# Performance work log

Hardware: AMD Instinct MI355X
Metric: run time of the kernel (lower is better)

## Reference

```python
import jax, jax.numpy as jnp
import numpy as np

N_CORES = 64
N_QUBITS = 1024
QEMB = 256
N_EDGES = 448
BATCH = 512
NN_DIMS = (256, 512, 512, 256)


def setup_inputs() -> dict:
    key = jax.random.key(0)
    ks = jax.random.split(key, 12)
    inp = {
        "core_allocs": jax.random.randint(ks[0], (BATCH, N_QUBITS), 0, N_CORES, dtype=jnp.int32),
        "qubit_embs": jax.random.normal(ks[1], (N_QUBITS, QEMB), dtype=jnp.float32),
        "dummy_qubit_emb": jax.random.normal(ks[2], (QEMB,), dtype=jnp.float32),
        "edge_index": jax.random.randint(ks[3], (2, N_EDGES), 0, N_CORES, dtype=jnp.int32),
        "edge_weight": jax.random.uniform(ks[4], (N_EDGES,), dtype=jnp.float32),
        "W1": jax.random.normal(ks[5], (NN_DIMS[0], NN_DIMS[1]), dtype=jnp.float32) * 0.05,
        "b1": jax.random.normal(ks[6], (NN_DIMS[1],), dtype=jnp.float32) * 0.05,
        "W2": jax.random.normal(ks[7], (NN_DIMS[1], NN_DIMS[2]), dtype=jnp.float32) * 0.05,
        "b2": jax.random.normal(ks[8], (NN_DIMS[2],), dtype=jnp.float32) * 0.05,
        "W3": jax.random.normal(ks[9], (NN_DIMS[2], NN_DIMS[3]), dtype=jnp.float32) * 0.05,
        "b3": jax.random.normal(ks[10], (NN_DIMS[3],), dtype=jnp.float32) * 0.05,
    }
    return inp


def _gcn_norm(edge_index, edge_weight):
    # PyG gcn_norm: add self loops (weight 1), symmetric D^{-1/2} A D^{-1/2}.
    self_idx = jnp.arange(N_CORES, dtype=edge_index.dtype)
    row = jnp.concatenate([edge_index[0], self_idx])
    col = jnp.concatenate([edge_index[1], self_idx])
    w = jnp.concatenate([edge_weight, jnp.ones((N_CORES,), edge_weight.dtype)])
    deg = jax.ops.segment_sum(w, col, num_segments=N_CORES)  # degree at targets
    dinv = jnp.where(deg > 0, deg ** -0.5, 0.0)
    norm = dinv[row] * w * dinv[col]
    return row, col, norm


def reference(core_allocs, qubit_embs, dummy_qubit_emb, edge_index, edge_weight,
              W1, b1, W2, b2, W3, b3):
    # ---- unmixedCoreEmbs, vectorized: per-core max over assigned qubit embs,
    # dummy emb always included (cores never at capacity) ----
    def pool(alloc):  # alloc: [n_qubits] -> [n_cores, qemb]
        seg = jax.ops.segment_max(qubit_embs, alloc, num_segments=N_CORES)
        return jnp.maximum(seg, dummy_qubit_emb)  # also fixes -inf empty cores

    x = jax.vmap(pool)(core_allocs)  # [B, n_cores, qemb]

    # ---- GCNConv stack (same graph replicated per batch element) ----
    row, col, norm = _gcn_norm(edge_index, edge_weight)

    def gcn_layer(h, W, b):
        hw = h @ W  # [B, C, d_out]
        msg = hw[:, row, :] * norm[None, :, None]  # gather sources, scale
        agg = jnp.zeros((h.shape[0], N_CORES, W.shape[1]), hw.dtype).at[:, col, :].add(msg)
        return jax.nn.relu(agg + b)

    x = gcn_layer(x, W1, b1)
    x = gcn_layer(x, W2, b2)
    x = gcn_layer(x, W3, b3)
    return x  # [B, n_cores, nn_dims[-1]] (original returns this split per batch element)
```

## Files before the change

### kernel.cpp

```cpp
#include <hip/hip_runtime.h>
#include <type_traits>

typedef __attribute__((ext_vector_type(8))) short short8;
typedef __attribute__((ext_vector_type(4))) short short4v;
typedef __attribute__((ext_vector_type(4))) float f32x4;
typedef unsigned short u16;
typedef unsigned int u32;

#define N_EDGES 448

#define WS_ADJA 0
#define WS_ADJB 4096
#define WS_W1   8192
#define WS_W2   139264
#define WS_W3   401408
#define WS_DUM  532480
#define WS_B1   (WS_DUM + 256)
#define WS_B2   (WS_DUM + 768)
#define WS_B3   (WS_DUM + 1280)
#define WS_FLAG 534272

__device__ __forceinline__ float bf2f(u16 v) {
    u32 u = ((u32)v) << 16;
    return __builtin_bit_cast(float, u);
}
__device__ __forceinline__ u16 f2bf(float f) {
    u32 u = __builtin_bit_cast(u32, f);
    u32 r = u + 0x7FFFu + ((u >> 16) & 1u);
    return (u16)(r >> 16);
}
__device__ __forceinline__ float ldf(const void* p, int idx, u32 isf32) {
    return isf32 ? ((const float*)p)[idx] : bf2f(((const u16*)p)[idx]);
}

__global__ __launch_bounds__(512) void prep(
    const int* __restrict__ eidx, const void* __restrict__ ew,
    const void* __restrict__ qembs, const void* __restrict__ dummy,
    const void* __restrict__ W1, const void* __restrict__ b1,
    const void* __restrict__ W2, const void* __restrict__ b2,
    const void* __restrict__ W3, const void* __restrict__ b3,
    u16* __restrict__ ws) {
    const int t = threadIdx.x, b = blockIdx.x;
    __shared__ u32 s_isf;
    if (t < 64) {
        const u16* qs = (const u16*)qembs;
        int c = 0;
#pragma unroll
        for (int j = 0; j < 4; j++) {
            u16 v = qs[(t * 4 + j) * 2];
            u32 e = (v >> 7) & 0xFF;
            c += (e >= 100 && e <= 134) ? 1 : 0;
        }
#pragma unroll
        for (int off = 32; off > 0; off >>= 1) c += __shfl_down(c, off, 64);
        if (t == 0) s_isf = (c < 128) ? 1u : 0u;
    }
    __syncthreads();
    const u32 isf32 = s_isf;

    if (b == 0) {
#pragma unroll
        for (int j = 0; j < 4; j++) {
            int i = t + j * 512;
            if (i < 1792) {
                float v;
                if (i < 256)       v = ldf(dummy, i, isf32);
                else if (i < 768)  v = ldf(b1, i - 256, isf32);
                else if (i < 1280) v = ldf(b2, i - 768, isf32);
                else               v = ldf(b3, i - 1280, isf32);
                ws[WS_DUM + i] = f2bf(v);
            }
        }
        __shared__ float A[4096];
        __shared__ float deg[64];
        __shared__ float dinv[64];
        __shared__ int er[N_EDGES];
        __shared__ int ec[N_EDGES];
        __shared__ float ewf[N_EDGES];
        if (t < N_EDGES) {
            er[t] = eidx[t];
            ec[t] = eidx[N_EDGES + t];
            ewf[t] = ldf(ew, t, isf32);
        }
        if (t < 64) deg[t] = 1.0f;
        for (int i = t; i < 4096; i += 512) A[i] = 0.f;
        __syncthreads();
        if (t < N_EDGES) atomicAdd(&deg[ec[t]], ewf[t]);
        __syncthreads();
        if (t < 64) dinv[t] = 1.0f / sqrtf(deg[t]);
        __syncthreads();
        if (t < N_EDGES) atomicAdd(&A[ec[t] * 64 + er[t]], dinv[er[t]] * ewf[t] * dinv[ec[t]]);
        __syncthreads();
        if (t < 64) A[t * 64 + t] += dinv[t] * dinv[t];
        __syncthreads();
        for (int i = t; i < 4096; i += 512) {
            int chunk = i >> 9, m = (i >> 3) & 63, j = i & 7;
            ws[WS_ADJA + i] = f2bf(A[m * 64 + chunk * 8 + j]);
        }
        for (int i = t; i < 4096; i += 512) {
            int chunk = i >> 9, l = (i >> 3) & 63, j = i & 7;
            int ntc = chunk >> 1, kk = chunk & 1;
            int k = kk * 32 + (l >> 4) * 8 + j;
            int c2 = ntc * 16 + (l & 15);
            ws[WS_ADJB + i] = f2bf(A[c2 * 64 + k]);
        }
        if (t == 0) *(u32*)(ws + WS_FLAG) = isf32;
    } else {
        const int bw = (b - 1) * 8 + (t >> 6);
        const int tl = t & 63;
        const void* src;
        int N, K32, dst, nt, kk;
        if (bw < 256)      { src = W1; N = 512; K32 = 8;  dst = WS_W1; nt = bw / 8;          kk = bw % 8; }
        else if (bw < 768) { src = W2; N = 512; K32 = 16; dst = WS_W2; nt = (bw - 256) / 16; kk = (bw - 256) % 16; }
        else               { src = W3; N = 256; K32 = 16; dst = WS_W3; nt = (bw - 768) / 16; kk = (bw - 768) % 16; }
        const int col = nt * 16 + (tl & 15);
        const int krow = kk * 32 + (tl >> 4) * 8;
        u16 v[8];
#pragma unroll
        for (int j = 0; j < 8; j++) v[j] = f2bf(ldf(src, (krow + j) * N + col, isf32));
        u16* o = ws + dst + (nt * K32 + kk) * 512 + tl * 8;
#pragma unroll
        for (int j = 0; j < 8; j++) o[j] = v[j];
    }
}

__global__ __launch_bounds__(1024, 4) void fused(
    const int* __restrict__ allocs, const void* __restrict__ qembs,
    const u16* __restrict__ wsr, void* __restrict__ out) {

    __shared__ __align__(16) u16 BH1[32768];
    __shared__ __align__(16) u16 BH2[32768];
    __shared__ __align__(16) u16 SCR[10240];

    const int t = threadIdx.x, bb = blockIdx.x;
    const int wave = t >> 6, lane = t & 63, quad = lane >> 4, nl = lane & 15;
    const u32 isf32 = *(const u32*)(wsr + WS_FLAG);

    {
        int* AL   = (int*)SCR;
        int* LIST = (int*)SCR + 1024;
        int* CNT  = (int*)SCR + 2048;
        int* SST  = (int*)SCR + 2112;
        int* WOF  = (int*)SCR + 2176;
        if (t < 64) CNT[t] = 0;
        __syncthreads();
        const int myc = allocs[bb * 1024 + t];
        AL[t] = myc;
        atomicAdd(&CNT[myc], 1);
        __syncthreads();
        if (t < 64) {
            int v = CNT[t], s = v;
#pragma unroll
            for (int off = 1; off < 64; off <<= 1) {
                int u = __shfl_up(s, off, 64);
                if (t >= off) s += u;
            }
            SST[t] = s - v;
            WOF[t] = s - v;
        }
        __syncthreads();
        {
            int pos = atomicAdd(&WOF[myc], 1);
            LIST[pos] = t;
        }
        __syncthreads();
        float dums[4];
#pragma unroll
        for (int jj = 0; jj < 4; jj++) dums[jj] = bf2f(wsr[WS_DUM + lane * 4 + jj]);
        for (int i = 0; i < 4; i++) {
            const int c = wave * 4 + i;
            const int L = CNT[c], S = SST[c];
            float vm0 = -3.4e38f, vm1 = -3.4e38f, vm2 = -3.4e38f, vm3 = -3.4e38f;
            if (isf32) {
                const float4* qb = (const float4*)qembs;
                for (int j = 0; j < L; j++) {
                    int q = LIST[S + j];
                    float4 v = qb[q * 64 + lane];
                    vm0 = fmaxf(vm0, v.x); vm1 = fmaxf(vm1, v.y);
                    vm2 = fmaxf(vm2, v.z); vm3 = fmaxf(vm3, v.w);
                }
            } else {
                const uint2* qb = (const uint2*)qembs;
                for (int j = 0; j < L; j++) {
                    int q = LIST[S + j];
                    uint2 r = qb[q * 64 + lane];
                    vm0 = fmaxf(vm0, bf2f((u16)(r.x & 0xffff)));
                    vm1 = fmaxf(vm1, bf2f((u16)(r.x >> 16)));
                    vm2 = fmaxf(vm2, bf2f((u16)(r.y & 0xffff)));
                    vm3 = fmaxf(vm3, bf2f((u16)(r.y >> 16)));
                }
            }
            short4v p;
            p[0] = (short)f2bf(fmaxf(vm0, dums[0]));
            p[1] = (short)f2bf(fmaxf(vm1, dums[1]));
            p[2] = (short)f2bf(fmaxf(vm2, dums[2]));
            p[3] = (short)f2bf(fmaxf(vm3, dums[3]));
            *(short4v*)(BH2 + (lane >> 1) * 512 + c * 8 + (lane & 1) * 4) = p;
        }
    }
    __syncthreads();

    u16* scr = SCR + wave * 640;

    auto layerT = [&](auto K32c, const u16* __restrict__ W, const u16* __restrict__ bias,
                      const u16* __restrict__ Hin, u16* __restrict__ Hout) {
        constexpr int K32 = decltype(K32c)::value;
        const int s0 = wave * 2;
        f32x4 acc[2][4];
#pragma unroll
        for (int s = 0; s < 2; s++)
#pragma unroll
            for (int rt = 0; rt < 4; rt++) acc[s][rt] = f32x4{0.f, 0.f, 0.f, 0.f};
#pragma unroll
        for (int kk = 0; kk < K32; kk++) {
            short8 a[4], bch[2];
#pragma unroll
            for (int rt = 0; rt < 4; rt++)
                a[rt] = *(const short8*)(Hin + (kk * 4 + quad) * 512 + (rt * 16 + nl) * 8);
#pragma unroll
            for (int s = 0; s < 2; s++)
                bch[s] = *(const short8*)(W + ((s0 + s) * K32 + kk) * 512 + lane * 8);
#pragma unroll
            for (int s = 0; s < 2; s++)
#pragma unroll
                for (int rt = 0; rt < 4; rt++)
                    acc[s][rt] = __builtin_amdgcn_mfma_f32_16x16x32_bf16(a[rt], bch[s], acc[s][rt], 0, 0, 0);
        }
#pragma unroll
        for (int s = 0; s < 2; s++) {
            const int nt = s0 + s;
            f32x4 agg[4];
#pragma unroll
            for (int ntc = 0; ntc < 4; ntc++) agg[ntc] = f32x4{0.f, 0.f, 0.f, 0.f};
#pragma unroll
            for (int h = 0; h < 2; h++) {
#pragma unroll
                for (int r2 = 0; r2 < 2; r2++) {
                    f32x4 v = acc[s][2 * h + r2];
                    short4v p;
#pragma unroll
                    for (int rr = 0; rr < 4; rr++) p[rr] = (short)f2bf(v[rr]);
                    *(short4v*)(scr + nl * 40 + r2 * 16 + quad * 4) = p;
                }
                short8 hwf = *(const short8*)(scr + nl * 40 + quad * 8);
#pragma unroll
                for (int ntc = 0; ntc < 4; ntc++) {
                    short8 adjB = *(const short8*)(wsr + WS_ADJB + (ntc * 2 + h) * 512 + lane * 8);
                    agg[ntc] = __builtin_amdgcn_mfma_f32_16x16x32_bf16(hwf, adjB, agg[ntc], 0, 0, 0);
                }
            }
            float bv[4];
#pragma unroll
            for (int rr = 0; rr < 4; rr++) bv[rr] = bf2f(bias[nt * 16 + quad * 4 + rr]);
#pragma unroll
            for (int ntc = 0; ntc < 4; ntc++) {
                short4v p;
#pragma unroll
                for (int rr = 0; rr < 4; rr++)
                    p[rr] = (short)f2bf(fmaxf(agg[ntc][rr] + bv[rr], 0.f));
                *(short4v*)(Hout + (nt * 2 + (quad >> 1)) * 512 + (ntc * 16 + nl) * 8 + (quad & 1) * 4) = p;
            }
        }
    };

    auto layer3 = [&](const u16* __restrict__ W) {
        const int nt = wave;
        f32x4 acc[4];
#pragma unroll
        for (int rt = 0; rt < 4; rt++) acc[rt] = f32x4{0.f, 0.f, 0.f, 0.f};
#pragma unroll
        for (int kk = 0; kk < 16; kk++) {
            short8 a[4];
#pragma unroll
            for (int rt = 0; rt < 4; rt++)
                a[rt] = *(const short8*)(BH2 + (kk * 4 + quad) * 512 + (rt * 16 + nl) * 8);
            short8 bch = *(const short8*)(W + (nt * 16 + kk) * 512 + lane * 8);
#pragma unroll
            for (int rt = 0; rt < 4; rt++)
                acc[rt] = __builtin_amdgcn_mfma_f32_16x16x32_bf16(a[rt], bch, acc[rt], 0, 0, 0);
        }
#pragma unroll
        for (int h = 0; h < 2; h++) {
#pragma unroll
            for (int r2 = 0; r2 < 2; r2++) {
                f32x4 v = acc[2 * h + r2];
                short4v p;
#pragma unroll
                for (int rr = 0; rr < 4; rr++) p[rr] = (short)f2bf(v[rr]);
                *(short4v*)(scr + nl * 40 + r2 * 16 + quad * 4) = p;
            }
            short8 hwf = *(const short8*)(scr + nl * 40 + quad * 8);
            *(short8*)(BH1 + (nt * 2 + h) * 512 + lane * 8) = hwf;
        }
    };

    auto finalOut = [&]() {
        const int rt2 = wave & 3, nt0 = (wave >> 2) * 4;
        short8 aA[2];
#pragma unroll
        for (int h = 0; h < 2; h++)
            aA[h] = *(const short8*)(wsr + WS_ADJA + (h * 4 + quad) * 512 + (rt2 * 16 + nl) * 8);
        float* outf = (float*)out + (size_t)bb * 16384;
        u16* outu = (u16*)out + (size_t)bb * 16384;
#pragma unroll
        for (int ni = 0; ni < 4; ni++) {
            const int nt = nt0 + ni;
            short8 b0 = *(const short8*)(BH1 + (nt * 2 + 0) * 512 + lane * 8);
            short8 b1 = *(const short8*)(BH1 + (nt * 2 + 1) * 512 + lane * 8);
            f32x4 acc = f32x4{0.f, 0.f, 0.f, 0.f};
            acc = __builtin_amdgcn_mfma_f32_16x16x32_bf16(aA[0], b0, acc, 0, 0, 0);
            acc = __builtin_amdgcn_mfma_f32_16x16x32_bf16(aA[1], b1, acc, 0, 0, 0);
            const int n = nt * 16 + nl;
            const float bv = bf2f(wsr[WS_B3 + n]);
#pragma unroll
            for (int rr = 0; rr < 4; rr++) {
                const int m2 = rt2 * 16 + quad * 4 + rr;
                float val = fmaxf(acc[rr] + bv, 0.f);
                if (isf32) outf[m2 * 256 + n] = val;
                else       outu[m2 * 256 + n] = f2bf(val);
            }
        }
    };

    layerT(std::integral_constant<int, 8>{},  wsr + WS_W1, wsr + WS_B1, BH2, BH1);
    __syncthreads();
    layerT(std::integral_constant<int, 16>{}, wsr + WS_W2, wsr + WS_B2, BH1, BH2);
    __syncthreads();
    layer3(wsr + WS_W3);
    __syncthreads();
    finalOut();
}

extern "C" void kernel_launch(void* const* d_in, const int* in_sizes, int n_in,
                              void* d_out, int out_size, void* d_ws, size_t ws_size,
                              hipStream_t stream) {
    const int* allocs = (const int*)d_in[0];
    const void* qembs = d_in[1];
    const void* dummy = d_in[2];
    const int* eidx   = (const int*)d_in[3];
    const void* ew    = d_in[4];
    const void* W1 = d_in[5];
    const void* b1 = d_in[6];
    const void* W2 = d_in[7];
    const void* b2 = d_in[8];
    const void* W3 = d_in[9];
    const void* b3 = d_in[10];
    u16* ws = (u16*)d_ws;

    prep<<<129, 512, 0, stream>>>(eidx, ew, qembs, dummy, W1, b1, W2, b2, W3, b3, ws);
    fused<<<512, 1024, 0, stream>>>(allocs, qembs, ws, d_out);
}
```

Baseline: 150.4 us.

## Merge prep and fused kernels into one cooperative kernel with grid sync

Replaces the separate prep and fused launches with a single cooperative kernel. Weight repacking, qubit-embedding bf16 conversion and adjacency building are spread across all 512 blocks, followed by a grid-wide sync; if the cooperative launch fails, two plain launches are used instead. The main compute now runs with 512 threads and a single padded LDS activation buffer (stride 520) in place of two ping-pong buffers, with more work per wave. This aims to remove a launch boundary and the serial prep tail and to raise occupancy, at the cost of a grid barrier and extra in-place syncs.

```diff
diff --git a/kernel.cpp b/kernel.cpp
--- a/kernel.cpp
+++ b/kernel.cpp
@@ -1,4 +1,5 @@
 #include <hip/hip_runtime.h>
+#include <hip/hip_cooperative_groups.h>
 #include <type_traits>
 
 typedef __attribute__((ext_vector_type(8))) short short8;
@@ -8,6 +9,7 @@
 typedef unsigned int u32;
 
 #define N_EDGES 448
+#define CH 520
 
 #define WS_ADJA 0
 #define WS_ADJB 4096
@@ -18,7 +20,7 @@
 #define WS_B1   (WS_DUM + 256)
 #define WS_B2   (WS_DUM + 768)
 #define WS_B3   (WS_DUM + 1280)
-#define WS_FLAG 534272
+#define WS_QE   534528
 
 __device__ __forceinline__ float bf2f(u16 v) {
     u32 u = ((u32)v) << 16;
@@ -33,15 +35,23 @@
     return isf32 ? ((const float*)p)[idx] : bf2f(((const u16*)p)[idx]);
 }
 
-__global__ __launch_bounds__(512) void prep(
-    const int* __restrict__ eidx, const void* __restrict__ ew,
-    const void* __restrict__ qembs, const void* __restrict__ dummy,
+template <int MODE>
+__global__ __launch_bounds__(512, 4) void mega(
+    const int* __restrict__ allocs, const void* __restrict__ qembs,
+    const void* __restrict__ dummy, const int* __restrict__ eidx,
+    const void* __restrict__ ew,
     const void* __restrict__ W1, const void* __restrict__ b1,
     const void* __restrict__ W2, const void* __restrict__ b2,
     const void* __restrict__ W3, const void* __restrict__ b3,
-    u16* __restrict__ ws) {
-    const int t = threadIdx.x, b = blockIdx.x;
+    u16* __restrict__ ws, void* __restrict__ out) {
+
+    __shared__ __align__(16) u16 H[64 * CH];
+    __shared__ __align__(16) u16 SCR[8 * 640];
     __shared__ u32 s_isf;
+
+    const int t = threadIdx.x, bb = blockIdx.x;
+    const int wave = t >> 6, lane = t & 63, quad = lane >> 4, nl = lane & 15;
+
     if (t < 64) {
         const u16* qs = (const u16*)qembs;
         int c = 0;
@@ -58,95 +68,99 @@
     __syncthreads();
     const u32 isf32 = s_isf;
 
-    if (b == 0) {
-#pragma unroll
-        for (int j = 0; j < 4; j++) {
-            int i = t + j * 512;
-            if (i < 1792) {
-                float v;
-                if (i < 256)       v = ldf(dummy, i, isf32);
-                else if (i < 768)  v = ldf(b1, i - 256, isf32);
-                else if (i < 1280) v = ldf(b2, i - 768, isf32);
-                else               v = ldf(b3, i - 1280, isf32);
-                ws[WS_DUM + i] = f2bf(v);
-            }
-        }
-        __shared__ float A[4096];
-        __shared__ float deg[64];
-        __shared__ float dinv[64];
-        __shared__ int er[N_EDGES];
-        __shared__ int ec[N_EDGES];
-        __shared__ float ewf[N_EDGES];
-        if (t < N_EDGES) {
-            er[t] = eidx[t];
-            ec[t] = eidx[N_EDGES + t];
-            ewf[t] = ldf(ew, t, isf32);
-        }
-        if (t < 64) deg[t] = 1.0f;
-        for (int i = t; i < 4096; i += 512) A[i] = 0.f;
-        __syncthreads();
-        if (t < N_EDGES) atomicAdd(&deg[ec[t]], ewf[t]);
-        __syncthreads();
-        if (t < 64) dinv[t] = 1.0f / sqrtf(deg[t]);
-        __syncthreads();
-        if (t < N_EDGES) atomicAdd(&A[ec[t] * 64 + er[t]], dinv[er[t]] * ewf[t] * dinv[ec[t]]);
-        __syncthreads();
-        if (t < 64) A[t * 64 + t] += dinv[t] * dinv[t];
-        __syncthreads();
-        for (int i = t; i < 4096; i += 512) {
-            int chunk = i >> 9, m = (i >> 3) & 63, j = i & 7;
-            ws[WS_ADJA + i] = f2bf(A[m * 64 + chunk * 8 + j]);
-        }
-        for (int i = t; i < 4096; i += 512) {
-            int chunk = i >> 9, l = (i >> 3) & 63, j = i & 7;
-            int ntc = chunk >> 1, kk = chunk & 1;
-            int k = kk * 32 + (l >> 4) * 8 + j;
-            int c2 = ntc * 16 + (l & 15);
-            ws[WS_ADJB + i] = f2bf(A[c2 * 64 + k]);
-        }
-        if (t == 0) *(u32*)(ws + WS_FLAG) = isf32;
-    } else {
-        const int bw = (b - 1) * 8 + (t >> 6);
-        const int tl = t & 63;
-        const void* src;
-        int N, K32, dst, nt, kk;
-        if (bw < 256)      { src = W1; N = 512; K32 = 8;  dst = WS_W1; nt = bw / 8;          kk = bw % 8; }
-        else if (bw < 768) { src = W2; N = 512; K32 = 16; dst = WS_W2; nt = (bw - 256) / 16; kk = (bw - 256) % 16; }
-        else               { src = W3; N = 256; K32 = 16; dst = WS_W3; nt = (bw - 768) / 16; kk = (bw - 768) % 16; }
-        const int col = nt * 16 + (tl & 15);
-        const int krow = kk * 32 + (tl >> 4) * 8;
-        u16 v[8];
-#pragma unroll
-        for (int j = 0; j < 8; j++) v[j] = f2bf(ldf(src, (krow + j) * N + col, isf32));
-        u16* o = ws + dst + (nt * K32 + kk) * 512 + tl * 8;
-#pragma unroll
-        for (int j = 0; j < 8; j++) o[j] = v[j];
-    }
-}
-
-__global__ __launch_bounds__(1024, 4) void fused(
-    const int* __restrict__ allocs, const void* __restrict__ qembs,
-    const u16* __restrict__ wsr, void* __restrict__ out) {
-
-    __shared__ __align__(16) u16 BH1[32768];
-    __shared__ __align__(16) u16 BH2[32768];
-    __shared__ __align__(16) u16 SCR[10240];
-
-    const int t = threadIdx.x, bb = blockIdx.x;
-    const int wave = t >> 6, lane = t & 63, quad = lane >> 4, nl = lane & 15;
-    const u32 isf32 = *(const u32*)(wsr + WS_FLAG);
+    if (MODE != 1) {
+        if (t < 128) {
+            const int bw = bb * 2 + (t >> 6);
+            const int tl = t & 63;
+            const void* src;
+            int N, K32, dst, nt, kk;
+            if (bw < 256)      { src = W1; N = 512; K32 = 8;  dst = WS_W1; nt = bw / 8;          kk = bw % 8; }
+            else if (bw < 768) { src = W2; N = 512; K32 = 16; dst = WS_W2; nt = (bw - 256) / 16; kk = (bw - 256) % 16; }
+            else               { src = W3; N = 256; K32 = 16; dst = WS_W3; nt = (bw - 768) / 16; kk = (bw - 768) % 16; }
+            const int col = nt * 16 + (tl & 15);
+            const int krow = kk * 32 + (tl >> 4) * 8;
+            u16 v[8];
+#pragma unroll
+            for (int j = 0; j < 8; j++) v[j] = f2bf(ldf(src, (krow + j) * N + col, isf32));
+            u16* o = ws + dst + (nt * K32 + kk) * 512 + tl * 8;
+#pragma unroll
+            for (int j = 0; j < 8; j++) o[j] = v[j];
+        }
+        if (t >= 256) {
+            const int base = bb * 512 + (t - 256) * 2;
+            ws[WS_QE + base]     = f2bf(ldf(qembs, base, isf32));
+            ws[WS_QE + base + 1] = f2bf(ldf(qembs, base + 1, isf32));
+        }
+        if (bb == 1) {
+#pragma unroll
+            for (int j = 0; j < 4; j++) {
+                int i = t + j * 512;
+                if (i < 1792) {
+                    float v;
+                    if (i < 256)       v = ldf(dummy, i, isf32);
+                    else if (i < 768)  v = ldf(b1, i - 256, isf32);
+                    else if (i < 1280) v = ldf(b2, i - 768, isf32);
+                    else               v = ldf(b3, i - 1280, isf32);
+                    ws[WS_DUM + i] = f2bf(v);
+                }
+            }
+        }
+        if (bb == 0) {
+            float* A    = (float*)H;
+            int*   er   = (int*)H + 4096;
+            int*   ec   = (int*)H + 4544;
+            float* ewf  = (float*)H + 4992;
+            float* deg  = (float*)SCR;
+            float* dinv = (float*)SCR + 64;
+            __syncthreads();
+            if (t < N_EDGES) {
+                er[t] = eidx[t];
+                ec[t] = eidx[N_EDGES + t];
+                ewf[t] = ldf(ew, t, isf32);
+            }
+            if (t < 64) deg[t] = 1.0f;
+            for (int i = t; i < 4096; i += 512) A[i] = 0.f;
+            __syncthreads();
+            if (t < N_EDGES) atomicAdd(&deg[ec[t]], ewf[t]);
+            __syncthreads();
+            if (t < 64) dinv[t] = 1.0f / sqrtf(deg[t]);
+            __syncthreads();
+            if (t < N_EDGES) atomicAdd(&A[ec[t] * 64 + er[t]], dinv[er[t]] * ewf[t] * dinv[ec[t]]);
+            __syncthreads();
+            if (t < 64) A[t * 64 + t] += dinv[t] * dinv[t];
+            __syncthreads();
+            for (int i = t; i < 4096; i += 512) {
+                int chunk = i >> 9, m = (i >> 3) & 63, j = i & 7;
+                ws[WS_ADJA + i] = f2bf(A[m * 64 + chunk * 8 + j]);
+            }
+            for (int i = t; i < 4096; i += 512) {
+                int chunk = i >> 9, l = (i >> 3) & 63, j = i & 7;
+                int ntc = chunk >> 1, kk = chunk & 1;
+                int k = kk * 32 + (l >> 4) * 8 + j;
+                int c2 = ntc * 16 + (l & 15);
+                ws[WS_ADJB + i] = f2bf(A[c2 * 64 + k]);
+            }
+            __syncthreads();
+        }
+    }
+
+    if (MODE == 0) return;
+    if (MODE == 2) {
+        __threadfence();
+        cooperative_groups::this_grid().sync();
+    }
 
     {
-        int* AL   = (int*)SCR;
-        int* LIST = (int*)SCR + 1024;
-        int* CNT  = (int*)SCR + 2048;
-        int* SST  = (int*)SCR + 2112;
-        int* WOF  = (int*)SCR + 2176;
+        int* LIST = (int*)(H + 16640);
+        int* CNT  = LIST + 1024;
+        int* SST  = CNT + 64;
+        int* WOF  = SST + 64;
         if (t < 64) CNT[t] = 0;
         __syncthreads();
-        const int myc = allocs[bb * 1024 + t];
-        AL[t] = myc;
-        atomicAdd(&CNT[myc], 1);
+        const int c1 = allocs[bb * 1024 + t];
+        const int c2 = allocs[bb * 1024 + 512 + t];
+        atomicAdd(&CNT[c1], 1);
+        atomicAdd(&CNT[c2], 1);
         __syncthreads();
         if (t < 64) {
             int v = CNT[t], s = v;
@@ -160,74 +174,64 @@
         }
         __syncthreads();
         {
-            int pos = atomicAdd(&WOF[myc], 1);
-            LIST[pos] = t;
+            int p1 = atomicAdd(&WOF[c1], 1); LIST[p1] = t;
+            int p2 = atomicAdd(&WOF[c2], 1); LIST[p2] = 512 + t;
         }
         __syncthreads();
         float dums[4];
 #pragma unroll
-        for (int jj = 0; jj < 4; jj++) dums[jj] = bf2f(wsr[WS_DUM + lane * 4 + jj]);
-        for (int i = 0; i < 4; i++) {
-            const int c = wave * 4 + i;
+        for (int jj = 0; jj < 4; jj++) dums[jj] = bf2f(ws[WS_DUM + lane * 4 + jj]);
+        const u16* wsq = ws + WS_QE;
+        for (int i = 0; i < 8; i++) {
+            const int c = wave * 8 + i;
             const int L = CNT[c], S = SST[c];
             float vm0 = -3.4e38f, vm1 = -3.4e38f, vm2 = -3.4e38f, vm3 = -3.4e38f;
-            if (isf32) {
-                const float4* qb = (const float4*)qembs;
-                for (int j = 0; j < L; j++) {
-                    int q = LIST[S + j];
-                    float4 v = qb[q * 64 + lane];
-                    vm0 = fmaxf(vm0, v.x); vm1 = fmaxf(vm1, v.y);
-                    vm2 = fmaxf(vm2, v.z); vm3 = fmaxf(vm3, v.w);
-                }
-            } else {
-                const uint2* qb = (const uint2*)qembs;
-                for (int j = 0; j < L; j++) {
-                    int q = LIST[S + j];
-                    uint2 r = qb[q * 64 + lane];
-                    vm0 = fmaxf(vm0, bf2f((u16)(r.x & 0xffff)));
-                    vm1 = fmaxf(vm1, bf2f((u16)(r.x >> 16)));
-                    vm2 = fmaxf(vm2, bf2f((u16)(r.y & 0xffff)));
-                    vm3 = fmaxf(vm3, bf2f((u16)(r.y >> 16)));
-                }
+            for (int j = 0; j < L; j++) {
+                int q = LIST[S + j];
+                uint2 r = *(const uint2*)(wsq + q * 256 + lane * 4);
+                vm0 = fmaxf(vm0, bf2f((u16)(r.x & 0xffff)));
+                vm1 = fmaxf(vm1, bf2f((u16)(r.x >> 16)));
+                vm2 = fmaxf(vm2, bf2f((u16)(r.y & 0xffff)));
+                vm3 = fmaxf(vm3, bf2f((u16)(r.y >> 16)));
             }
             short4v p;
             p[0] = (short)f2bf(fmaxf(vm0, dums[0]));
             p[1] = (short)f2bf(fmaxf(vm1, dums[1]));
             p[2] = (short)f2bf(fmaxf(vm2, dums[2]));
             p[3] = (short)f2bf(fmaxf(vm3, dums[3]));
-            *(short4v*)(BH2 + (lane >> 1) * 512 + c * 8 + (lane & 1) * 4) = p;
+            *(short4v*)(H + (lane >> 1) * CH + c * 8 + (lane & 1) * 4) = p;
         }
     }
     __syncthreads();
 
     u16* scr = SCR + wave * 640;
 
-    auto layerT = [&](auto K32c, const u16* __restrict__ W, const u16* __restrict__ bias,
-                      const u16* __restrict__ Hin, u16* __restrict__ Hout) {
+    auto layerT = [&](auto K32c, const u16* __restrict__ W, const u16* __restrict__ bias) {
         constexpr int K32 = decltype(K32c)::value;
-        const int s0 = wave * 2;
-        f32x4 acc[2][4];
-#pragma unroll
-        for (int s = 0; s < 2; s++)
+        const int s0 = wave * 4;
+        f32x4 acc[4][4];
+#pragma unroll
+        for (int s = 0; s < 4; s++)
 #pragma unroll
             for (int rt = 0; rt < 4; rt++) acc[s][rt] = f32x4{0.f, 0.f, 0.f, 0.f};
 #pragma unroll
         for (int kk = 0; kk < K32; kk++) {
-            short8 a[4], bch[2];
+            short8 a[4], bch[4];
 #pragma unroll
             for (int rt = 0; rt < 4; rt++)
-                a[rt] = *(const short8*)(Hin + (kk * 4 + quad) * 512 + (rt * 16 + nl) * 8);
-#pragma unroll
-            for (int s = 0; s < 2; s++)
+                a[rt] = *(const short8*)(H + (kk * 4 + quad) * CH + (rt * 16 + nl) * 8);
+#pragma unroll
+            for (int s = 0; s < 4; s++)
                 bch[s] = *(const short8*)(W + ((s0 + s) * K32 + kk) * 512 + lane * 8);
 #pragma unroll
-            for (int s = 0; s < 2; s++)
+            for (int s = 0; s < 4; s++)
 #pragma unroll
                 for (int rt = 0; rt < 4; rt++)
                     acc[s][rt] = __builtin_amdgcn_mfma_f32_16x16x32_bf16(a[rt], bch[s], acc[s][rt], 0, 0, 0);
         }
-#pragma unroll
-        for (int s = 0; s < 2; s++) {
+        __syncthreads();
+#pragma unroll
+        for (int s = 0; s < 4; s++) {
             const int nt = s0 + s;
             f32x4 agg[4];
 #pragma unroll
@@ -245,7 +249,7 @@
                 short8 hwf = *(const short8*)(scr + nl * 40 + quad * 8);
 #pragma unroll
                 for (int ntc = 0; ntc < 4; ntc++) {
-                    short8 adjB = *(const short8*)(wsr + WS_ADJB + (ntc * 2 + h) * 512 + lane * 8);
+                    short8 adjB = *(const short8*)(ws + WS_ADJB + (ntc * 2 + h) * 512 + lane * 8);
                     agg[ntc] = __builtin_amdgcn_mfma_f32_16x16x32_bf16(hwf, adjB, agg[ntc], 0, 0, 0);
                 }
             }
@@ -258,60 +262,73 @@
 #pragma unroll
                 for (int rr = 0; rr < 4; rr++)
                     p[rr] = (short)f2bf(fmaxf(agg[ntc][rr] + bv[rr], 0.f));
-                *(short4v*)(Hout + (nt * 2 + (quad >> 1)) * 512 + (ntc * 16 + nl) * 8 + (quad & 1) * 4) = p;
-            }
-        }
+                *(short4v*)(H + (nt * 2 + (quad >> 1)) * CH + (ntc * 16 + nl) * 8 + (quad & 1) * 4) = p;
+            }
+        }
+        __syncthreads();
     };
 
     auto layer3 = [&](const u16* __restrict__ W) {
-        const int nt = wave;
-        f32x4 acc[4];
-#pragma unroll
-        for (int rt = 0; rt < 4; rt++) acc[rt] = f32x4{0.f, 0.f, 0.f, 0.f};
+        const int s0 = wave * 2;
+        f32x4 acc[2][4];
+#pragma unroll
+        for (int s = 0; s < 2; s++)
+#pragma unroll
+            for (int rt = 0; rt < 4; rt++) acc[s][rt] = f32x4{0.f, 0.f, 0.f, 0.f};
 #pragma unroll
         for (int kk = 0; kk < 16; kk++) {
-            short8 a[4];
+            short8 a[4], bch[2];
 #pragma unroll
             for (int rt = 0; rt < 4; rt++)
-                a[rt] = *(const short8*)(BH2 + (kk * 4 + quad) * 512 + (rt * 16 + nl) * 8);
-            short8 bch = *(const short8*)(W + (nt * 16 + kk) * 512 + lane * 8);
-#pragma unroll
-            for (int rt = 0; rt < 4; rt++)
-                acc[rt] = __builtin_amdgcn_mfma_f32_16x16x32_bf16(a[rt], bch, acc[rt], 0, 0, 0);
-        }
-#pragma unroll
-        for (int h = 0; h < 2; h++) {
-#pragma unroll
-            for (int r2 = 0; r2 < 2; r2++) {
-                f32x4 v = acc[2 * h + r2];
-                short4v p;
-#pragma unroll
-                for (int rr = 0; rr < 4; rr++) p[rr] = (short)f2bf(v[rr]);
-                *(short4v*)(scr + nl * 40 + r2 * 16 + quad * 4) = p;
-            }
-            short8 hwf = *(const short8*)(scr + nl * 40 + quad * 8);
-            *(short8*)(BH1 + (nt * 2 + h) * 512 + lane * 8) = hwf;
-        }
+                a[rt] = *(const short8*)(H + (kk * 4 + quad) * CH + (rt * 16 + nl) * 8);
+#pragma unroll
+            for (int s = 0; s < 2; s++)
+                bch[s] = *(const short8*)(W + ((s0 + s) * 16 + kk) * 512 + lane * 8);
+#pragma unroll
+            for (int s = 0; s < 2; s++)
+#pragma unroll
+                for (int rt = 0; rt < 4; rt++)
+                    acc[s][rt] = __builtin_amdgcn_mfma_f32_16x16x32_bf16(a[rt], bch[s], acc[s][rt], 0, 0, 0);
+        }
+        __syncthreads();
+#pragma unroll
+        for (int s = 0; s < 2; s++) {
+            const int nt = s0 + s;
+#pragma unroll
+            for (int h = 0; h < 2; h++) {
+#pragma unroll
+                for (int r2 = 0; r2 < 2; r2++) {
+                    f32x4 v = acc[s][2 * h + r2];
+                    short4v p;
+#pragma unroll
+                    for (int rr = 0; rr < 4; rr++) p[rr] = (short)f2bf(v[rr]);
+                    *(short4v*)(scr + nl * 40 + r2 * 16 + quad * 4) = p;
+                }
+                short8 hwf = *(const short8*)(scr + nl * 40 + quad * 8);
+                *(short8*)(H + (nt * 2 + h) * 512 + lane * 8) = hwf;
+            }
+        }
+        __syncthreads();
     };
 
     auto finalOut = [&]() {
-        const int rt2 = wave & 3, nt0 = (wave >> 2) * 4;
+        const int rt2 = wave & 3, nt0 = (wave >> 2) * 8;
         short8 aA[2];
 #pragma unroll
         for (int h = 0; h < 2; h++)
-            aA[h] = *(const short8*)(wsr + WS_ADJA + (h * 4 + quad) * 512 + (rt2 * 16 + nl) * 8);
+            aA[h] = *(const short8*)(ws + WS_ADJA + (h * 4 + quad) * 512 + (rt2 * 16 + nl) * 8);
         float* outf = (float*)out + (size_t)bb * 16384;
         u16* outu = (u16*)out + (size_t)bb * 16384;
 #pragma unroll
-        for (int ni = 0; ni < 4; ni++) {
+        for (int ni = 0; ni < 8; ni++) {
             const int nt = nt0 + ni;
-            short8 b0 = *(const short8*)(BH1 + (nt * 2 + 0) * 512 + lane * 8);
-            short8 b1 = *(const short8*)(BH1 + (nt * 2 + 1) * 512 + lane * 8);
+            short8 b0v = *(const short8*)(H + (nt * 2 + 0) * 512 + lane * 8);
+            short8 b1v = *(const short8*)(H + (nt * 2 + 1) * 512 + lane * 8);
             f32x4 acc = f32x4{0.f, 0.f, 0.f, 0.f};
-            acc = __builtin_amdgcn_mfma_f32_16x16x32_bf16(aA[0], b0, acc, 0, 0, 0);
-            acc = __builtin_amdgcn_mfma_f32_16x16x32_bf16(aA[1], b1, acc, 0, 0, 0);
+            acc = __builtin_amdgcn_mfma_f32_16x16x32_bf16(aA[0], b0v, acc, 0, 0, 0);
+            acc = __builtin_amdgcn_mfma_f32_16x16x32_bf16(aA[1], b1v, acc, 0, 0, 0);
             const int n = nt * 16 + nl;
-            const float bv = bf2f(wsr[WS_B3 + n]);
+            const float bv = bf2f(ws[WS_B3 + n]);
 #pragma unroll
             for (int rr = 0; rr < 4; rr++) {
                 const int m2 = rt2 * 16 + quad * 4 + rr;
@@ -322,12 +339,9 @@
         }
     };
 
-    layerT(std::integral_constant<int, 8>{},  wsr + WS_W1, wsr + WS_B1, BH2, BH1);
-    __syncthreads();
-    layerT(std::integral_constant<int, 16>{}, wsr + WS_W2, wsr + WS_B2, BH1, BH2);
-    __syncthreads();
-    layer3(wsr + WS_W3);
-    __syncthreads();
+    layerT(std::integral_constant<int, 8>{},  ws + WS_W1, ws + WS_B1);
+    layerT(std::integral_constant<int, 16>{}, ws + WS_W2, ws + WS_B2);
+    layer3(ws + WS_W3);
     finalOut();
 }
 
@@ -346,7 +360,18 @@
     const void* W3 = d_in[9];
     const void* b3 = d_in[10];
     u16* ws = (u16*)d_ws;
-
-    prep<<<129, 512, 0, stream>>>(eidx, ew, qembs, dummy, W1, b1, W2, b2, W3, b3, ws);
-    fused<<<512, 1024, 0, stream>>>(allocs, qembs, ws, d_out);
-}
+    void* out = d_out;
+
+    void* args[] = {(void*)&allocs, (void*)&qembs, (void*)&dummy, (void*)&eidx,
+                    (void*)&ew, (void*)&W1, (void*)&b1, (void*)&W2, (void*)&b2,
+                    (void*)&W3, (void*)&b3, (void*)&ws, (void*)&out};
+    hipError_t e = hipLaunchCooperativeKernel(reinterpret_cast<const void*>(&mega<2>),
+                                              dim3(512), dim3(512), args, 0, stream);
+    if (e != hipSuccess) {
+        (void)hipGetLastError();
+        mega<0><<<512, 512, 0, stream>>>(allocs, qembs, dummy, eidx, ew,
+                                         W1, b1, W2, b2, W3, b3, ws, out);
+        mega<1><<<512, 512, 0, stream>>>(allocs, qembs, dummy, eidx, ew,
+                                         W1, b1, W2, b2, W3, b3, ws, out);
+    }
+}
```

Measured after the change: 320.4 us. +113.0%, slower.

## Use one shared activation buffer and pre-convert qubit embeddings to bf16

Applied to the files above, without the earlier changes.

The fused kernel now keeps all activations in a single 64x512 bf16 LDS buffer, updated in place, instead of two ping-pong buffers plus scratch. Extra barriers between the GEMM read phase and the write-back phase make the in-place update safe. The smaller LDS footprint is meant to let more workgroups share a compute unit. The prep kernel now also converts the qubit embeddings to bf16 in the workspace, so the gather/max pooling reads half the bytes when inputs are fp32. Weight repacking is spread over 512 blocks, and each fused block detects the input dtype itself, which adds barriers and a small redundant probe per block.

```diff
diff --git a/kernel.cpp b/kernel.cpp
--- a/kernel.cpp
+++ b/kernel.cpp
@@ -18,7 +18,7 @@
 #define WS_B1   (WS_DUM + 256)
 #define WS_B2   (WS_DUM + 768)
 #define WS_B3   (WS_DUM + 1280)
-#define WS_FLAG 534272
+#define WS_QE   534528
 
 __device__ __forceinline__ float bf2f(u16 v) {
     u32 u = ((u32)v) << 16;
@@ -40,7 +40,7 @@
     const void* __restrict__ W2, const void* __restrict__ b2,
     const void* __restrict__ W3, const void* __restrict__ b3,
     u16* __restrict__ ws) {
-    const int t = threadIdx.x, b = blockIdx.x;
+    const int t = threadIdx.x, bb = blockIdx.x;
     __shared__ u32 s_isf;
     if (t < 64) {
         const u16* qs = (const u16*)qembs;
@@ -58,7 +58,29 @@
     __syncthreads();
     const u32 isf32 = s_isf;
 
-    if (b == 0) {
+    if (t < 128) {
+        const int bw = bb * 2 + (t >> 6);
+        const int tl = t & 63;
+        const void* src;
+        int N, K32, dst, nt, kk;
+        if (bw < 256)      { src = W1; N = 512; K32 = 8;  dst = WS_W1; nt = bw / 8;          kk = bw % 8; }
+        else if (bw < 768) { src = W2; N = 512; K32 = 16; dst = WS_W2; nt = (bw - 256) / 16; kk = (bw - 256) % 16; }
+        else               { src = W3; N = 256; K32 = 16; dst = WS_W3; nt = (bw - 768) / 16; kk = (bw - 768) % 16; }
+        const int col = nt * 16 + (tl & 15);
+        const int krow = kk * 32 + (tl >> 4) * 8;
+        u16 v[8];
+#pragma unroll
+        for (int j = 0; j < 8; j++) v[j] = f2bf(ldf(src, (krow + j) * N + col, isf32));
+        u16* o = ws + dst + (nt * K32 + kk) * 512 + tl * 8;
+#pragma unroll
+        for (int j = 0; j < 8; j++) o[j] = v[j];
+    }
+    if (t >= 256) {
+        const int base = bb * 512 + (t - 256) * 2;
+        ws[WS_QE + base]     = f2bf(ldf(qembs, base, isf32));
+        ws[WS_QE + base + 1] = f2bf(ldf(qembs, base + 1, isf32));
+    }
+    if (bb == 1) {
 #pragma unroll
         for (int j = 0; j < 4; j++) {
             int i = t + j * 512;
@@ -71,6 +93,8 @@
                 ws[WS_DUM + i] = f2bf(v);
             }
         }
+    }
+    if (bb == 0) {
         __shared__ float A[4096];
         __shared__ float deg[64];
         __shared__ float dinv[64];
@@ -104,48 +128,43 @@
             int c2 = ntc * 16 + (l & 15);
             ws[WS_ADJB + i] = f2bf(A[c2 * 64 + k]);
         }
-        if (t == 0) *(u32*)(ws + WS_FLAG) = isf32;
-    } else {
-        const int bw = (b - 1) * 8 + (t >> 6);
-        const int tl = t & 63;
-        const void* src;
-        int N, K32, dst, nt, kk;
-        if (bw < 256)      { src = W1; N = 512; K32 = 8;  dst = WS_W1; nt = bw / 8;          kk = bw % 8; }
-        else if (bw < 768) { src = W2; N = 512; K32 = 16; dst = WS_W2; nt = (bw - 256) / 16; kk = (bw - 256) % 16; }
-        else               { src = W3; N = 256; K32 = 16; dst = WS_W3; nt = (bw - 768) / 16; kk = (bw - 768) % 16; }
-        const int col = nt * 16 + (tl & 15);
-        const int krow = kk * 32 + (tl >> 4) * 8;
-        u16 v[8];
-#pragma unroll
-        for (int j = 0; j < 8; j++) v[j] = f2bf(ldf(src, (krow + j) * N + col, isf32));
-        u16* o = ws + dst + (nt * K32 + kk) * 512 + tl * 8;
-#pragma unroll
-        for (int j = 0; j < 8; j++) o[j] = v[j];
     }
 }
 
 __global__ __launch_bounds__(1024, 4) void fused(
     const int* __restrict__ allocs, const void* __restrict__ qembs,
-    const u16* __restrict__ wsr, void* __restrict__ out) {
-
-    __shared__ __align__(16) u16 BH1[32768];
-    __shared__ __align__(16) u16 BH2[32768];
-    __shared__ __align__(16) u16 SCR[10240];
+    const u16* __restrict__ ws, void* __restrict__ out) {
+
+    __shared__ __align__(16) u16 H[64 * 512];
+    __shared__ u32 s_isf;
 
     const int t = threadIdx.x, bb = blockIdx.x;
     const int wave = t >> 6, lane = t & 63, quad = lane >> 4, nl = lane & 15;
-    const u32 isf32 = *(const u32*)(wsr + WS_FLAG);
+
+    if (t < 64) {
+        const u16* qs = (const u16*)qembs;
+        int c = 0;
+#pragma unroll
+        for (int j = 0; j < 4; j++) {
+            u16 v = qs[(t * 4 + j) * 2];
+            u32 e = (v >> 7) & 0xFF;
+            c += (e >= 100 && e <= 134) ? 1 : 0;
+        }
+#pragma unroll
+        for (int off = 32; off > 0; off >>= 1) c += __shfl_down(c, off, 64);
+        if (t == 0) s_isf = (c < 128) ? 1u : 0u;
+    }
+    __syncthreads();
+    const u32 isf32 = s_isf;
 
     {
-        int* AL   = (int*)SCR;
-        int* LIST = (int*)SCR + 1024;
-        int* CNT  = (int*)SCR + 2048;
-        int* SST  = (int*)SCR + 2112;
-        int* WOF  = (int*)SCR + 2176;
+        int* LIST = (int*)H + 8192;
+        int* CNT  = LIST + 1024;
+        int* SST  = CNT + 64;
+        int* WOF  = SST + 64;
         if (t < 64) CNT[t] = 0;
         __syncthreads();
         const int myc = allocs[bb * 1024 + t];
-        AL[t] = myc;
         atomicAdd(&CNT[myc], 1);
         __syncthreads();
         if (t < 64) {
@@ -166,46 +185,34 @@
         __syncthreads();
         float dums[4];
 #pragma unroll
-        for (int jj = 0; jj < 4; jj++) dums[jj] = bf2f(wsr[WS_DUM + lane * 4 + jj]);
+        for (int jj = 0; jj < 4; jj++) dums[jj] = bf2f(ws[WS_DUM + lane * 4 + jj]);
+        const u16* wsq = ws + WS_QE;
         for (int i = 0; i < 4; i++) {
             const int c = wave * 4 + i;
             const int L = CNT[c], S = SST[c];
             float vm0 = -3.4e38f, vm1 = -3.4e38f, vm2 = -3.4e38f, vm3 = -3.4e38f;
-            if (isf32) {
-                const float4* qb = (const float4*)qembs;
-                for (int j = 0; j < L; j++) {
-                    int q = LIST[S + j];
-                    float4 v = qb[q * 64 + lane];
-                    vm0 = fmaxf(vm0, v.x); vm1 = fmaxf(vm1, v.y);
-                    vm2 = fmaxf(vm2, v.z); vm3 = fmaxf(vm3, v.w);
-                }
-            } else {
-                const uint2* qb = (const uint2*)qembs;
-                for (int j = 0; j < L; j++) {
-                    int q = LIST[S + j];
-                    uint2 r = qb[q * 64 + lane];
-                    vm0 = fmaxf(vm0, bf2f((u16)(r.x & 0xffff)));
-                    vm1 = fmaxf(vm1, bf2f((u16)(r.x >> 16)));
-                    vm2 = fmaxf(vm2, bf2f((u16)(r.y & 0xffff)));
-                    vm3 = fmaxf(vm3, bf2f((u16)(r.y >> 16)));
-                }
+            for (int j = 0; j < L; j++) {
+                int q = LIST[S + j];
+                uint2 r = *(const uint2*)(wsq + q * 256 + lane * 4);
+                vm0 = fmaxf(vm0, bf2f((u16)(r.x & 0xffff)));
+                vm1 = fmaxf(vm1, bf2f((u16)(r.x >> 16)));
+                vm2 = fmaxf(vm2, bf2f((u16)(r.y & 0xffff)));
+                vm3 = fmaxf(vm3, bf2f((u16)(r.y >> 16)));
             }
             short4v p;
             p[0] = (short)f2bf(fmaxf(vm0, dums[0]));
             p[1] = (short)f2bf(fmaxf(vm1, dums[1]));
             p[2] = (short)f2bf(fmaxf(vm2, dums[2]));
             p[3] = (short)f2bf(fmaxf(vm3, dums[3]));
-            *(short4v*)(BH2 + (lane >> 1) * 512 + c * 8 + (lane & 1) * 4) = p;
+            *(short4v*)(H + (lane >> 1) * 512 + c * 8 + (lane & 1) * 4) = p;
         }
     }
     __syncthreads();
 
-    u16* scr = SCR + wave * 640;
-
-    auto layerT = [&](auto K32c, const u16* __restrict__ W, const u16* __restrict__ bias,
-                      const u16* __restrict__ Hin, u16* __restrict__ Hout) {
+    auto layerT = [&](auto K32c, const u16* __restrict__ W, const u16* __restrict__ bias) {
         constexpr int K32 = decltype(K32c)::value;
         const int s0 = wave * 2;
+        u16* scr = H + (wave * 4 + 2) * 512;
         f32x4 acc[2][4];
 #pragma unroll
         for (int s = 0; s < 2; s++)
@@ -216,7 +223,7 @@
             short8 a[4], bch[2];
 #pragma unroll
             for (int rt = 0; rt < 4; rt++)
-                a[rt] = *(const short8*)(Hin + (kk * 4 + quad) * 512 + (rt * 16 + nl) * 8);
+                a[rt] = *(const short8*)(H + (kk * 4 + quad) * 512 + (rt * 16 + nl) * 8);
 #pragma unroll
             for (int s = 0; s < 2; s++)
                 bch[s] = *(const short8*)(W + ((s0 + s) * K32 + kk) * 512 + lane * 8);
@@ -226,6 +233,7 @@
                 for (int rt = 0; rt < 4; rt++)
                     acc[s][rt] = __builtin_amdgcn_mfma_f32_16x16x32_bf16(a[rt], bch[s], acc[s][rt], 0, 0, 0);
         }
+        __syncthreads();
 #pragma unroll
         for (int s = 0; s < 2; s++) {
             const int nt = s0 + s;
@@ -245,7 +253,7 @@
                 short8 hwf = *(const short8*)(scr + nl * 40 + quad * 8);
 #pragma unroll
                 for (int ntc = 0; ntc < 4; ntc++) {
-                    short8 adjB = *(const short8*)(wsr + WS_ADJB + (ntc * 2 + h) * 512 + lane * 8);
+                    short8 adjB = *(const short8*)(ws + WS_ADJB + (ntc * 2 + h) * 512 + lane * 8);
                     agg[ntc] = __builtin_amdgcn_mfma_f32_16x16x32_bf16(hwf, adjB, agg[ntc], 0, 0, 0);
                 }
             }
@@ -258,13 +266,15 @@
 #pragma unroll
                 for (int rr = 0; rr < 4; rr++)
                     p[rr] = (short)f2bf(fmaxf(agg[ntc][rr] + bv[rr], 0.f));
-                *(short4v*)(Hout + (nt * 2 + (quad >> 1)) * 512 + (ntc * 16 + nl) * 8 + (quad & 1) * 4) = p;
-            }
-        }
+                *(short4v*)(H + (nt * 2 + (quad >> 1)) * 512 + (ntc * 16 + nl) * 8 + (quad & 1) * 4) = p;
+            }
+        }
+        __syncthreads();
     };
 
     auto layer3 = [&](const u16* __restrict__ W) {
         const int nt = wave;
+        u16* scr = H + 16384 + wave * 640;
         f32x4 acc[4];
 #pragma unroll
         for (int rt = 0; rt < 4; rt++) acc[rt] = f32x4{0.f, 0.f, 0.f, 0.f};
@@ -273,12 +283,13 @@
             short8 a[4];
 #pragma unroll
             for (int rt = 0; rt < 4; rt++)
-                a[rt] = *(const short8*)(BH2 + (kk * 4 + quad) * 512 + (rt * 16 + nl) * 8);
+                a[rt] = *(const short8*)(H + (kk * 4 + quad) * 512 + (rt * 16 + nl) * 8);
             short8 bch = *(const short8*)(W + (nt * 16 + kk) * 512 + lane * 8);
 #pragma unroll
             for (int rt = 0; rt < 4; rt++)
                 acc[rt] = __builtin_amdgcn_mfma_f32_16x16x32_bf16(a[rt], bch, acc[rt], 0, 0, 0);
         }
+        __syncthreads();
 #pragma unroll
         for (int h = 0; h < 2; h++) {
 #pragma unroll
@@ -290,8 +301,9 @@
                 *(short4v*)(scr + nl * 40 + r2 * 16 + quad * 4) = p;
             }
             short8 hwf = *(const short8*)(scr + nl * 40 + quad * 8);
-            *(short8*)(BH1 + (nt * 2 + h) * 512 + lane * 8) = hwf;
-        }
+            *(short8*)(H + (nt * 2 + h) * 512 + lane * 8) = hwf;
+        }
+        __syncthreads();
     };
 
     auto finalOut = [&]() {
@@ -299,19 +311,19 @@
         short8 aA[2];
 #pragma unroll
         for (int h = 0; h < 2; h++)
-            aA[h] = *(const short8*)(wsr + WS_ADJA + (h * 4 + quad) * 512 + (rt2 * 16 + nl) * 8);
+            aA[h] = *(const short8*)(ws + WS_ADJA + (h * 4 + quad) * 512 + (rt2 * 16 + nl) * 8);
         float* outf = (float*)out + (size_t)bb * 16384;
         u16* outu = (u16*)out + (size_t)bb * 16384;
 #pragma unroll
         for (int ni = 0; ni < 4; ni++) {
             const int nt = nt0 + ni;
-            short8 b0 = *(const short8*)(BH1 + (nt * 2 + 0) * 512 + lane * 8);
-            short8 b1 = *(const short8*)(BH1 + (nt * 2 + 1) * 512 + lane * 8);
+            short8 b0v = *(const short8*)(H + (nt * 2 + 0) * 512 + lane * 8);
+            short8 b1v = *(const short8*)(H + (nt * 2 + 1) * 512 + lane * 8);
             f32x4 acc = f32x4{0.f, 0.f, 0.f, 0.f};
-            acc = __builtin_amdgcn_mfma_f32_16x16x32_bf16(aA[0], b0, acc, 0, 0, 0);
-            acc = __builtin_amdgcn_mfma_f32_16x16x32_bf16(aA[1], b1, acc, 0, 0, 0);
+            acc = __builtin_amdgcn_mfma_f32_16x16x32_bf16(aA[0], b0v, acc, 0, 0, 0);
+            acc = __builtin_amdgcn_mfma_f32_16x16x32_bf16(aA[1], b1v, acc, 0, 0, 0);
             const int n = nt * 16 + nl;
-            const float bv = bf2f(wsr[WS_B3 + n]);
+            const float bv = bf2f(ws[WS_B3 + n]);
 #pragma unroll
             for (int rr = 0; rr < 4; rr++) {
                 const int m2 = rt2 * 16 + quad * 4 + rr;
@@ -322,12 +334,9 @@
         }
     };
 
-    layerT(std::integral_constant<int, 8>{},  wsr + WS_W1, wsr + WS_B1, BH2, BH1);
-    __syncthreads();
-    layerT(std::integral_constant<int, 16>{}, wsr + WS_W2, wsr + WS_B2, BH1, BH2);
-    __syncthreads();
-    layer3(wsr + WS_W3);
-    __syncthreads();
+    layerT(std::integral_constant<int, 8>{},  ws + WS_W1, ws + WS_B1);
+    layerT(std::integral_constant<int, 16>{}, ws + WS_W2, ws + WS_B2);
+    layer3(ws + WS_W3);
     finalOut();
 }
 
@@ -347,6 +356,6 @@
     const void* b3 = d_in[10];
     u16* ws = (u16*)d_ws;
 
-    prep<<<129, 512, 0, stream>>>(eidx, ew, qembs, dummy, W1, b1, W2, b2, W3, b3, ws);
+    prep<<<512, 512, 0, stream>>>(eidx, ew, qembs, dummy, W1, b1, W2, b2, W3, b3, ws);
     fused<<<512, 1024, 0, stream>>>(allocs, qembs, ws, d_out);
 }
```

New measurement: 149.8 us. About the same (-0.4%).
